# Kernel optimization log

Measured on AMD Instinct MI355X. Metric: run time of the kernel, lower is better.

The kernel has to match this reference:

```python
import jax, jax.numpy as jnp
import numpy as np


def setup_inputs() -> dict:
    key = jax.random.key(0)
    ks = jax.random.split(key, 6)
    B, S, I, H = 8, 4096, 512, 512
    scale = 1.0 / np.sqrt(I)
    return {
        "x": jax.random.normal(ks[0], (B, S, I), dtype=jnp.float32),
        "h_0": jax.random.normal(ks[1], (B, H), dtype=jnp.float32),
        "W_z": jax.random.normal(ks[2], (H, I), dtype=jnp.float32) * scale,
        "b_z": jax.random.normal(ks[3], (H,), dtype=jnp.float32) * scale,
        "W_h": jax.random.normal(ks[4], (H, I), dtype=jnp.float32) * scale,
        "b_h": jax.random.normal(ks[5], (H,), dtype=jnp.float32) * scale,
    }


def reference(x, h_0, W_z, b_z, W_h, b_h):
    # Gate and candidate projections (dense GEMMs over all timesteps at once)
    z = jax.nn.sigmoid(jnp.einsum("bsi,hi->bsh", x, W_z) + b_z)  # [B,S,H]
    h_tilde = jnp.einsum("bsi,hi->bsh", x, W_h) + b_h            # [B,S,H]

    # Linear recurrence h_t = a_t * h_{t-1} + b_t with a = 1-z, b = z*h_tilde.
    # Parallel associative scan over time; h_0 folded in as element 0 (a=1, b=h_0).
    a = jnp.concatenate([jnp.ones_like(h_0)[:, None, :], 1.0 - z], axis=1)     # [B,S+1,H]
    b = jnp.concatenate([h_0[:, None, :], z * h_tilde], axis=1)                # [B,S+1,H]

    def combine(c1, c2):
        a1, b1 = c1
        a2, b2 = c2
        return a1 * a2, a2 * b1 + b2

    _, h = jax.lax.associative_scan(combine, (a, b), axis=1)
    return h[:, 1:, :]  # drop the h_0 slot -> [B,S,H]
```

## Files before the change

kernel.cpp:

```cpp
#include <hip/hip_runtime.h>
#include <hip/hip_bf16.h>
#include <stdint.h>


typedef __attribute__((ext_vector_type(8))) short short8;
typedef __attribute__((ext_vector_type(4))) float f32x4;

#define AS1 __attribute__((address_space(1)))
#define AS3 __attribute__((address_space(3)))

__device__ inline void gload_lds16(const void* g, void* l) {
  __builtin_amdgcn_global_load_lds((AS1 uint32_t*)(g), (AS3 uint32_t*)(l), 16, 0, 0);
}

__device__ inline ushort f2bf(float f) {
  union { __hip_bfloat16 h; ushort u; } v;
  v.h = __float2bfloat16(f);
  return v.u;
}

__global__ void cvt_all(const float* __restrict__ x,
                        const float* __restrict__ wz,
                        const float* __restrict__ wh,
                        ushort* __restrict__ xb,
                        ushort* __restrict__ wzb,
                        ushort* __restrict__ whb) {
  int i = blockIdx.x * 256 + threadIdx.x;
  for (; i < 4325376; i += 2048 * 256) {
    const float* s; ushort* d; int j;
    if (i < 4194304)      { s = x;  d = xb;  j = i; }
    else if (i < 4259840) { s = wz; d = wzb; j = i - 4194304; }
    else                  { s = wh; d = whb; j = i - 4259840; }
    float4 v = reinterpret_cast<const float4*>(s)[j];
    ushort4 o = make_ushort4(f2bf(v.x), f2bf(v.y), f2bf(v.z), f2bf(v.w));
    reinterpret_cast<ushort4*>(d)[j] = o;
  }
}

__global__ __launch_bounds__(256) void gemm_gate(
    const ushort* __restrict__ xb,
    const ushort* __restrict__ wzb,
    const ushort* __restrict__ whb,
    const float* __restrict__ b_z,
    const float* __restrict__ b_h,
    uint* __restrict__ ab,
    float2* __restrict__ ABc)
{
  __shared__ __align__(16) char smem[32768];
  char* As  = smem;
  char* Bzs = smem + 16384;
  char* Bhs = smem + 24576;

  const int t  = threadIdx.x;
  const int w  = t >> 6;
  const int l  = t & 63;
  const int lm = l & 15;
  const int lk = l >> 4;
  const int wm = w >> 1, wn = w & 1;
  const int bx = blockIdx.x;
  const int m0 = bx * 128;
  const int n0 = blockIdx.y * 64;

  const int srow  = t >> 3;
  const int sslot = t & 7;

  float bzv[2], bhv[2];
  #pragma unroll
  for (int n = 0; n < 2; ++n) {
    int col = n0 + wn * 32 + n * 16 + lm;
    bzv[n] = b_z[col];
    bhv[n] = b_h[col];
  }

  f32x4 accz[4][2], acch[4][2];
  #pragma unroll
  for (int m = 0; m < 4; ++m)
    #pragma unroll
    for (int n = 0; n < 2; ++n) {
      accz[m][n] = (f32x4){0.f, 0.f, 0.f, 0.f};
      acch[m][n] = (f32x4){0.f, 0.f, 0.f, 0.f};
    }

  for (int kt = 0; kt < 8; ++kt) {
    const int k0 = kt * 64;
    #pragma unroll
    for (int j = 0; j < 4; ++j) {
      int row = j * 32 + srow;
      int gs  = sslot ^ (row & 7);
      gload_lds16(xb + (size_t)(m0 + row) * 512 + k0 + gs * 8, As + j * 4096 + w * 1024);
    }
    #pragma unroll
    for (int j = 0; j < 2; ++j) {
      int row = j * 32 + srow;
      int gs  = sslot ^ (row & 7);
      gload_lds16(wzb + (size_t)(n0 + row) * 512 + k0 + gs * 8, Bzs + j * 4096 + w * 1024);
      gload_lds16(whb + (size_t)(n0 + row) * 512 + k0 + gs * 8, Bhs + j * 4096 + w * 1024);
    }
    __syncthreads();

    #pragma unroll
    for (int kk = 0; kk < 2; ++kk) {
      short8 af[4], bfz[2], bfh[2];
      const int soff = (((kk * 4 + lk) ^ (lm & 7)) << 4);
      #pragma unroll
      for (int m = 0; m < 4; ++m) {
        int row = wm * 64 + m * 16 + lm;
        af[m] = *(const short8*)(As + row * 128 + soff);
      }
      #pragma unroll
      for (int n = 0; n < 2; ++n) {
        int row = wn * 32 + n * 16 + lm;
        bfz[n] = *(const short8*)(Bzs + row * 128 + soff);
        bfh[n] = *(const short8*)(Bhs + row * 128 + soff);
      }
      #pragma unroll
      for (int m = 0; m < 4; ++m)
        #pragma unroll
        for (int n = 0; n < 2; ++n) {
          accz[m][n] = __builtin_amdgcn_mfma_f32_16x16x32_bf16(af[m], bfz[n], accz[m][n], 0, 0, 0);
          acch[m][n] = __builtin_amdgcn_mfma_f32_16x16x32_bf16(af[m], bfh[n], acch[m][n], 0, 0, 0);
        }
    }
    __syncthreads();
  }

  float av[4][4][2], bv[4][4][2];
  #pragma unroll
  for (int m = 0; m < 4; ++m) {
    #pragma unroll
    for (int j = 0; j < 4; ++j) {
      size_t grow = (size_t)(m0 + wm * 64 + m * 16 + lk * 4 + j);
      uint* po = ab + grow * 512 + n0 + wn * 32 + lm;
      #pragma unroll
      for (int n = 0; n < 2; ++n) {
        float uz = accz[m][n][j] + bzv[n];
        float uh = acch[m][n][j] + bhv[n];
        float z  = 1.f / (1.f + __expf(-uz));
        float a  = 1.f - z;
        float bb = z * uh;
        av[m][j][n] = a;
        bv[m][j][n] = bb;
        po[n * 16] = (uint)f2bf(a) | ((uint)f2bf(bb) << 16);
      }
    }
  }

  #pragma unroll
  for (int cb = 0; cb < 2; ++cb) {
    #pragma unroll
    for (int n = 0; n < 2; ++n) {
      float At[2], Bt[2];
      #pragma unroll
      for (int mm = 0; mm < 2; ++mm) {
        float A = 1.f, Bv = 0.f;
        #pragma unroll
        for (int j = 0; j < 4; ++j) {
          float a = av[2 * cb + mm][j][n];
          float b = bv[2 * cb + mm][j][n];
          A  = a * A;
          Bv = a * Bv + b;
        }
        float Ag = 1.f, Bg = 0.f;
        #pragma unroll
        for (int q = 0; q < 4; ++q) {
          float Aq = __shfl(A,  lm + 16 * q);
          float Bq = __shfl(Bv, lm + 16 * q);
          Ag = Aq * Ag;
          Bg = Aq * Bg + Bq;
        }
        At[mm] = Ag;
        Bt[mm] = Bg;
      }
      float Achunk = At[1] * At[0];
      float Bchunk = At[1] * Bt[0] + Bt[1];
      if (lk == 0) {
        int bidx = bx >> 5;
        int c    = (bx & 31) * 4 + wm * 2 + cb;
        int col  = n0 + wn * 32 + n * 16 + lm;
        ABc[((size_t)bidx * 512 + col) * 128 + c] = make_float2(Achunk, Bchunk);
      }
    }
  }
}

__global__ __launch_bounds__(256) void chunk_scan(
    const float2* __restrict__ ABc,
    const float* __restrict__ h0,
    float* __restrict__ Hinit)
{
  __shared__ float sm[128][4];
  const int w = threadIdx.x >> 6, l = threadIdx.x & 63;
  const int b   = blockIdx.x >> 7;
  const int h0g = (blockIdx.x & 127) * 4;
  const int h   = h0g + w;

  const float2* base = ABc + ((size_t)b * 512 + h) * 128;
  float2 s1 = base[l];
  float2 s2 = base[64 + l];

  float A1 = s1.x, B1 = s1.y;
  #pragma unroll
  for (int d = 1; d < 64; d <<= 1) {
    float uA = __shfl_up(A1, d);
    float uB = __shfl_up(B1, d);
    if (l >= d) { B1 = A1 * uB + B1; A1 = A1 * uA; }
  }
  float A2 = s2.x, B2 = s2.y;
  #pragma unroll
  for (int d = 1; d < 64; d <<= 1) {
    float uA = __shfl_up(A2, d);
    float uB = __shfl_up(B2, d);
    if (l >= d) { B2 = A2 * uB + B2; A2 = A2 * uA; }
  }
  float PA = __shfl(A1, 63), PB = __shfl(B1, 63);
  float FA = A2 * PA;
  float FB = A2 * PB + B2;

  float e1A = __shfl_up(A1, 1), e1B = __shfl_up(B1, 1);
  if (l == 0) { e1A = 1.f; e1B = 0.f; }
  float e2A = __shfl_up(FA, 1), e2B = __shfl_up(FB, 1);
  if (l == 0) { e2A = PA; e2B = PB; }

  float h0v = h0[b * 512 + h];
  sm[l][w]      = e1A * h0v + e1B;
  sm[64 + l][w] = e2A * h0v + e2B;
  __syncthreads();

  const int t = threadIdx.x;
  if (t < 128) {
    float4 v = *(const float4*)sm[t];
    *(float4*)(Hinit + ((size_t)b * 128 + t) * 512 + h0g) = v;
  }
}

__global__ __launch_bounds__(256) void scan_write(
    const uint* __restrict__ ab,
    const float* __restrict__ Hinit,
    float* __restrict__ out)
{
  int tid = blockIdx.x * 256 + threadIdx.x;
  int cg = tid & 127;
  int c  = (tid >> 7) & 127;
  int b  = tid >> 14;
  const uint4* p = reinterpret_cast<const uint4*>(ab + ((size_t)(b * 4096 + c * 32)) * 512) + cg;
  float4 hv = *reinterpret_cast<const float4*>(Hinit + ((size_t)b * 128 + c) * 512 + cg * 4);
  float4* po = reinterpret_cast<float4*>(out + ((size_t)(b * 4096 + c * 32)) * 512) + cg;
  #pragma unroll 4
  for (int t = 0; t < 32; ++t) {
    uint4 u = p[(size_t)t * 128];
    hv.x = __uint_as_float(u.x << 16) * hv.x + __uint_as_float(u.x & 0xffff0000u);
    hv.y = __uint_as_float(u.y << 16) * hv.y + __uint_as_float(u.y & 0xffff0000u);
    hv.z = __uint_as_float(u.z << 16) * hv.z + __uint_as_float(u.z & 0xffff0000u);
    hv.w = __uint_as_float(u.w << 16) * hv.w + __uint_as_float(u.w & 0xffff0000u);
    po[(size_t)t * 128] = hv;
  }
}

extern "C" void kernel_launch(void* const* d_in, const int* in_sizes, int n_in,
                              void* d_out, int out_size, void* d_ws, size_t ws_size,
                              hipStream_t stream) {
  const float* x   = (const float*)d_in[0];
  const float* h0  = (const float*)d_in[1];
  const float* W_z = (const float*)d_in[2];
  const float* b_z = (const float*)d_in[3];
  const float* W_h = (const float*)d_in[4];
  const float* b_h = (const float*)d_in[5];
  float* out = (float*)d_out;

  char* ws = (char*)d_ws;
  ushort* xb    = (ushort*)(ws);
  ushort* wzb   = (ushort*)(ws + 33554432);
  ushort* whb   = (ushort*)(ws + 34078720);
  uint*   ab    = (uint*)  (ws + 34603008);
  float2* ABc   = (float2*)(ws + 101711872);
  float*  Hinit = (float*) (ws + 105906176);

  cvt_all<<<2048, 256, 0, stream>>>(x, W_z, W_h, xb, wzb, whb);
  gemm_gate<<<dim3(256, 8), 256, 0, stream>>>(xb, wzb, whb, b_z, b_h, ab, ABc);
  chunk_scan<<<1024, 256, 0, stream>>>(ABc, h0, Hinit);
  scan_write<<<512, 256, 0, stream>>>(ab, Hinit, out);
}
```

Measured before the change: 103.4 us.

## Double-buffer gate GEMM LDS tiles with K=32 stages and async prefetch

Reworks the gate/candidate GEMM main loop to double-buffer shared memory, using 16 stages of K=32 instead of 8 stages of K=64. The next tile is prefetched with global_load_lds while MFMAs run on the current one, synchronised by explicit vmcnt waits and raw barriers. It also raises wave priority around the MFMA block and changes the swizzle to suit the 64-byte rows. The aim is to hide global-to-LDS latency, at the cost of more barriers per K and reliance on hand-tuned waitcnt counts for correctness.

```diff
diff --git a/kernel.cpp b/kernel.cpp
--- a/kernel.cpp
+++ b/kernel.cpp
@@ -47,9 +47,6 @@
     float2* __restrict__ ABc)
 {
   __shared__ __align__(16) char smem[32768];
-  char* As  = smem;
-  char* Bzs = smem + 16384;
-  char* Bhs = smem + 24576;
 
   const int t  = threadIdx.x;
   const int w  = t >> 6;
@@ -61,8 +58,76 @@
   const int m0 = bx * 128;
   const int n0 = blockIdx.y * 64;
 
-  const int srow  = t >> 3;
-  const int sslot = t & 7;
+  const int srow = t >> 2;
+  const int ssl  = t & 3;
+
+  f32x4 accz[4][2], acch[4][2];
+  #pragma unroll
+  for (int m = 0; m < 4; ++m)
+    #pragma unroll
+    for (int n = 0; n < 2; ++n) {
+      accz[m][n] = (f32x4){0.f, 0.f, 0.f, 0.f};
+      acch[m][n] = (f32x4){0.f, 0.f, 0.f, 0.f};
+    }
+
+  auto stage = [&](int sel, int kt) {
+    char* base = smem + sel * 16384;
+    const int k0 = kt * 32;
+    #pragma unroll
+    for (int j = 0; j < 2; ++j) {
+      int row = j * 64 + srow;
+      int gs  = ssl ^ ((row >> 1) & 3);
+      gload_lds16(xb + (size_t)(m0 + row) * 512 + k0 + gs * 8,
+                  base + j * 4096 + w * 1024);
+    }
+    {
+      int row = srow;
+      int gs  = ssl ^ ((row >> 1) & 3);
+      gload_lds16(wzb + (size_t)(n0 + row) * 512 + k0 + gs * 8,
+                  base + 8192 + w * 1024);
+      gload_lds16(whb + (size_t)(n0 + row) * 512 + k0 + gs * 8,
+                  base + 12288 + w * 1024);
+    }
+  };
+
+  stage(0, 0);
+
+  #pragma unroll
+  for (int kt = 0; kt < 16; ++kt) {
+    const int sel = kt & 1;
+    if (kt < 15) {
+      stage(sel ^ 1, kt + 1);
+      asm volatile("s_waitcnt vmcnt(4)" ::: "memory");
+    } else {
+      asm volatile("s_waitcnt vmcnt(0)" ::: "memory");
+    }
+    __builtin_amdgcn_s_barrier();
+
+    const char* base = smem + sel * 16384;
+    short8 af[4], bfz[2], bfh[2];
+    #pragma unroll
+    for (int m = 0; m < 4; ++m) {
+      int row = wm * 64 + m * 16 + lm;
+      af[m] = *(const short8*)(base + row * 64 + ((lk ^ ((row >> 1) & 3)) << 4));
+    }
+    #pragma unroll
+    for (int n = 0; n < 2; ++n) {
+      int row = wn * 32 + n * 16 + lm;
+      int so  = ((lk ^ ((row >> 1) & 3)) << 4);
+      bfz[n] = *(const short8*)(base + 8192  + row * 64 + so);
+      bfh[n] = *(const short8*)(base + 12288 + row * 64 + so);
+    }
+    __builtin_amdgcn_s_setprio(1);
+    #pragma unroll
+    for (int m = 0; m < 4; ++m)
+      #pragma unroll
+      for (int n = 0; n < 2; ++n) {
+        accz[m][n] = __builtin_amdgcn_mfma_f32_16x16x32_bf16(af[m], bfz[n], accz[m][n], 0, 0, 0);
+        acch[m][n] = __builtin_amdgcn_mfma_f32_16x16x32_bf16(af[m], bfh[n], acch[m][n], 0, 0, 0);
+      }
+    __builtin_amdgcn_s_setprio(0);
+    __builtin_amdgcn_s_barrier();
+  }
 
   float bzv[2], bhv[2];
   #pragma unroll
@@ -70,58 +135,6 @@
     int col = n0 + wn * 32 + n * 16 + lm;
     bzv[n] = b_z[col];
     bhv[n] = b_h[col];
-  }
-
-  f32x4 accz[4][2], acch[4][2];
-  #pragma unroll
-  for (int m = 0; m < 4; ++m)
-    #pragma unroll
-    for (int n = 0; n < 2; ++n) {
-      accz[m][n] = (f32x4){0.f, 0.f, 0.f, 0.f};
-      acch[m][n] = (f32x4){0.f, 0.f, 0.f, 0.f};
-    }
-
-  for (int kt = 0; kt < 8; ++kt) {
-    const int k0 = kt * 64;
-    #pragma unroll
-    for (int j = 0; j < 4; ++j) {
-      int row = j * 32 + srow;
-      int gs  = sslot ^ (row & 7);
-      gload_lds16(xb + (size_t)(m0 + row) * 512 + k0 + gs * 8, As + j * 4096 + w * 1024);
-    }
-    #pragma unroll
-    for (int j = 0; j < 2; ++j) {
-      int row = j * 32 + srow;
-      int gs  = sslot ^ (row & 7);
-      gload_lds16(wzb + (size_t)(n0 + row) * 512 + k0 + gs * 8, Bzs + j * 4096 + w * 1024);
-      gload_lds16(whb + (size_t)(n0 + row) * 512 + k0 + gs * 8, Bhs + j * 4096 + w * 1024);
-    }
-    __syncthreads();
-
-    #pragma unroll
-    for (int kk = 0; kk < 2; ++kk) {
-      short8 af[4], bfz[2], bfh[2];
-      const int soff = (((kk * 4 + lk) ^ (lm & 7)) << 4);
-      #pragma unroll
-      for (int m = 0; m < 4; ++m) {
-        int row = wm * 64 + m * 16 + lm;
-        af[m] = *(const short8*)(As + row * 128 + soff);
-      }
-      #pragma unroll
-      for (int n = 0; n < 2; ++n) {
-        int row = wn * 32 + n * 16 + lm;
-        bfz[n] = *(const short8*)(Bzs + row * 128 + soff);
-        bfh[n] = *(const short8*)(Bhs + row * 128 + soff);
-      }
-      #pragma unroll
-      for (int m = 0; m < 4; ++m)
-        #pragma unroll
-        for (int n = 0; n < 2; ++n) {
-          accz[m][n] = __builtin_amdgcn_mfma_f32_16x16x32_bf16(af[m], bfz[n], accz[m][n], 0, 0, 0);
-          acch[m][n] = __builtin_amdgcn_mfma_f32_16x16x32_bf16(af[m], bfh[n], acch[m][n], 0, 0, 0);
-        }
-    }
-    __syncthreads();
   }
 
   float av[4][4][2], bv[4][4][2];
@@ -226,10 +239,10 @@
   sm[64 + l][w] = e2A * h0v + e2B;
   __syncthreads();
 
-  const int t = threadIdx.x;
-  if (t < 128) {
-    float4 v = *(const float4*)sm[t];
-    *(float4*)(Hinit + ((size_t)b * 128 + t) * 512 + h0g) = v;
+  const int tt = threadIdx.x;
+  if (tt < 128) {
+    float4 v = *(const float4*)sm[tt];
+    *(float4*)(Hinit + ((size_t)b * 128 + tt) * 512 + h0g) = v;
   }
 }
 
```

New measurement: 99.00 us. 1.04x faster.

## Rewrite gate GEMM as single-wave blocks loading operands directly from global

Applied to the files above, without the earlier changes.

The gate GEMM no longer stages tiles through LDS with global_load_lds and barriers. Each 64-thread block computes a 64x64 tile for both projections, reading MFMA operands straight from global memory into registers with double-buffered prefetch across K. Block IDs are remapped so neighbouring blocks share column tiles for cache locality. This drops LDS traffic and sync overhead but relies on L1/L2 for reuse, issues uncoalesced per-lane 16-byte loads, and raises register pressure from 32 accumulators plus two operand buffers.

```diff
diff --git a/kernel.cpp b/kernel.cpp
--- a/kernel.cpp
+++ b/kernel.cpp
@@ -5,13 +5,6 @@
 
 typedef __attribute__((ext_vector_type(8))) short short8;
 typedef __attribute__((ext_vector_type(4))) float f32x4;
-
-#define AS1 __attribute__((address_space(1)))
-#define AS3 __attribute__((address_space(3)))
-
-__device__ inline void gload_lds16(const void* g, void* l) {
-  __builtin_amdgcn_global_load_lds((AS1 uint32_t*)(g), (AS3 uint32_t*)(l), 16, 0, 0);
-}
 
 __device__ inline ushort f2bf(float f) {
   union { __hip_bfloat16 h; ushort u; } v;
@@ -37,7 +30,7 @@
   }
 }
 
-__global__ __launch_bounds__(256) void gemm_gate(
+__global__ __launch_bounds__(64) void gemm_gate(
     const ushort* __restrict__ xb,
     const ushort* __restrict__ wzb,
     const ushort* __restrict__ whb,
@@ -46,95 +39,86 @@
     uint* __restrict__ ab,
     float2* __restrict__ ABc)
 {
-  __shared__ __align__(16) char smem[32768];
-  char* As  = smem;
-  char* Bzs = smem + 16384;
-  char* Bhs = smem + 24576;
-
-  const int t  = threadIdx.x;
-  const int w  = t >> 6;
-  const int l  = t & 63;
+  const int l  = threadIdx.x;
   const int lm = l & 15;
   const int lk = l >> 4;
-  const int wm = w >> 1, wn = w & 1;
-  const int bx = blockIdx.x;
-  const int m0 = bx * 128;
-  const int n0 = blockIdx.y * 64;
-
-  const int srow  = t >> 3;
-  const int sslot = t & 7;
-
-  float bzv[2], bhv[2];
-  #pragma unroll
-  for (int n = 0; n < 2; ++n) {
-    int col = n0 + wn * 32 + n * 16 + lm;
+
+  const int bid  = blockIdx.x;
+  const int tile = (bid & 7) * 512 + (bid >> 3);
+  const int bx = tile >> 3;
+  const int by = tile & 7;
+  const int m0 = bx * 64;
+  const int n0 = by * 64;
+
+  const int lane_off = lm * 512 + lk * 8;
+
+  const ushort* ap[4];
+  const ushort* bp[8];
+  #pragma unroll
+  for (int m = 0; m < 4; ++m)
+    ap[m] = xb + (size_t)(m0 + m * 16) * 512 + lane_off;
+  #pragma unroll
+  for (int n = 0; n < 4; ++n) {
+    bp[n]     = wzb + (size_t)(n0 + n * 16) * 512 + lane_off;
+    bp[4 + n] = whb + (size_t)(n0 + n * 16) * 512 + lane_off;
+  }
+
+  f32x4 acc[2][4][4];
+  #pragma unroll
+  for (int q = 0; q < 2; ++q)
+    #pragma unroll
+    for (int m = 0; m < 4; ++m)
+      #pragma unroll
+      for (int n = 0; n < 4; ++n)
+        acc[q][m][n] = (f32x4){0.f, 0.f, 0.f, 0.f};
+
+  short8 aA[4], bA[8], aB[4], bB[8];
+
+#define LOADT(av_, bv_, ktv)                                         \
+  _Pragma("unroll") for (int m = 0; m < 4; ++m)                      \
+    av_[m] = *(const short8*)(ap[m] + (ktv) * 32);                   \
+  _Pragma("unroll") for (int q = 0; q < 8; ++q)                      \
+    bv_[q] = *(const short8*)(bp[q] + (ktv) * 32);
+
+#define COMPUTE(av_, bv_)                                            \
+  _Pragma("unroll") for (int m = 0; m < 4; ++m)                      \
+    _Pragma("unroll") for (int n = 0; n < 4; ++n) {                  \
+      acc[0][m][n] = __builtin_amdgcn_mfma_f32_16x16x32_bf16(        \
+          av_[m], bv_[n], acc[0][m][n], 0, 0, 0);                    \
+      acc[1][m][n] = __builtin_amdgcn_mfma_f32_16x16x32_bf16(        \
+          av_[m], bv_[4 + n], acc[1][m][n], 0, 0, 0);                \
+    }
+
+  LOADT(aA, bA, 0);
+  #pragma unroll
+  for (int kt = 0; kt < 16; kt += 2) {
+    LOADT(aB, bB, kt + 1);
+    COMPUTE(aA, bA);
+    if (kt + 2 < 16) { LOADT(aA, bA, kt + 2); }
+    COMPUTE(aB, bB);
+  }
+#undef LOADT
+#undef COMPUTE
+
+  float bzv[4], bhv[4];
+  #pragma unroll
+  for (int n = 0; n < 4; ++n) {
+    int col = n0 + n * 16 + lm;
     bzv[n] = b_z[col];
     bhv[n] = b_h[col];
   }
 
-  f32x4 accz[4][2], acch[4][2];
-  #pragma unroll
-  for (int m = 0; m < 4; ++m)
-    #pragma unroll
-    for (int n = 0; n < 2; ++n) {
-      accz[m][n] = (f32x4){0.f, 0.f, 0.f, 0.f};
-      acch[m][n] = (f32x4){0.f, 0.f, 0.f, 0.f};
-    }
-
-  for (int kt = 0; kt < 8; ++kt) {
-    const int k0 = kt * 64;
-    #pragma unroll
-    for (int j = 0; j < 4; ++j) {
-      int row = j * 32 + srow;
-      int gs  = sslot ^ (row & 7);
-      gload_lds16(xb + (size_t)(m0 + row) * 512 + k0 + gs * 8, As + j * 4096 + w * 1024);
-    }
-    #pragma unroll
-    for (int j = 0; j < 2; ++j) {
-      int row = j * 32 + srow;
-      int gs  = sslot ^ (row & 7);
-      gload_lds16(wzb + (size_t)(n0 + row) * 512 + k0 + gs * 8, Bzs + j * 4096 + w * 1024);
-      gload_lds16(whb + (size_t)(n0 + row) * 512 + k0 + gs * 8, Bhs + j * 4096 + w * 1024);
-    }
-    __syncthreads();
-
-    #pragma unroll
-    for (int kk = 0; kk < 2; ++kk) {
-      short8 af[4], bfz[2], bfh[2];
-      const int soff = (((kk * 4 + lk) ^ (lm & 7)) << 4);
-      #pragma unroll
-      for (int m = 0; m < 4; ++m) {
-        int row = wm * 64 + m * 16 + lm;
-        af[m] = *(const short8*)(As + row * 128 + soff);
-      }
-      #pragma unroll
-      for (int n = 0; n < 2; ++n) {
-        int row = wn * 32 + n * 16 + lm;
-        bfz[n] = *(const short8*)(Bzs + row * 128 + soff);
-        bfh[n] = *(const short8*)(Bhs + row * 128 + soff);
-      }
-      #pragma unroll
-      for (int m = 0; m < 4; ++m)
-        #pragma unroll
-        for (int n = 0; n < 2; ++n) {
-          accz[m][n] = __builtin_amdgcn_mfma_f32_16x16x32_bf16(af[m], bfz[n], accz[m][n], 0, 0, 0);
-          acch[m][n] = __builtin_amdgcn_mfma_f32_16x16x32_bf16(af[m], bfh[n], acch[m][n], 0, 0, 0);
-        }
-    }
-    __syncthreads();
-  }
-
-  float av[4][4][2], bv[4][4][2];
+  float av[4][4][4], bv[4][4][4];
   #pragma unroll
   for (int m = 0; m < 4; ++m) {
     #pragma unroll
     for (int j = 0; j < 4; ++j) {
-      size_t grow = (size_t)(m0 + wm * 64 + m * 16 + lk * 4 + j);
-      uint* po = ab + grow * 512 + n0 + wn * 32 + lm;
+      size_t grow = (size_t)(m0 + m * 16 + lk * 4 + j);
+      uint* po = ab + grow * 512 + n0 + lm;
       #pragma unroll
-      for (int n = 0; n < 2; ++n) {
-        float uz = accz[m][n][j] + bzv[n];
-        float uh = acch[m][n][j] + bhv[n];
+      for (int n = 0; n < 4; ++n) {
+        float uz = acc[0][m][n][j] + bzv[n];
+        float uh = acc[1][m][n][j] + bhv[n];
         float z  = 1.f / (1.f + __expf(-uz));
         float a  = 1.f - z;
         float bb = z * uh;
@@ -148,7 +132,7 @@
   #pragma unroll
   for (int cb = 0; cb < 2; ++cb) {
     #pragma unroll
-    for (int n = 0; n < 2; ++n) {
+    for (int n = 0; n < 4; ++n) {
       float At[2], Bt[2];
       #pragma unroll
       for (int mm = 0; mm < 2; ++mm) {
@@ -174,9 +158,9 @@
       float Achunk = At[1] * At[0];
       float Bchunk = At[1] * Bt[0] + Bt[1];
       if (lk == 0) {
-        int bidx = bx >> 5;
-        int c    = (bx & 31) * 4 + wm * 2 + cb;
-        int col  = n0 + wn * 32 + n * 16 + lm;
+        int bidx = bx >> 6;
+        int c    = (bx & 63) * 2 + cb;
+        int col  = n0 + n * 16 + lm;
         ABc[((size_t)bidx * 512 + col) * 128 + c] = make_float2(Achunk, Bchunk);
       }
     }
@@ -226,10 +210,10 @@
   sm[64 + l][w] = e2A * h0v + e2B;
   __syncthreads();
 
-  const int t = threadIdx.x;
-  if (t < 128) {
-    float4 v = *(const float4*)sm[t];
-    *(float4*)(Hinit + ((size_t)b * 128 + t) * 512 + h0g) = v;
+  const int tt = threadIdx.x;
+  if (tt < 128) {
+    float4 v = *(const float4*)sm[tt];
+    *(float4*)(Hinit + ((size_t)b * 128 + tt) * 512 + h0g) = v;
   }
 }
 
@@ -276,7 +260,7 @@
   float*  Hinit = (float*) (ws + 105906176);
 
   cvt_all<<<2048, 256, 0, stream>>>(x, W_z, W_h, xb, wzb, whb);
-  gemm_gate<<<dim3(256, 8), 256, 0, stream>>>(xb, wzb, whb, b_z, b_h, ab, ABc);
+  gemm_gate<<<4096, 64, 0, stream>>>(xb, wzb, whb, b_z, b_h, ab, ABc);
   chunk_scan<<<1024, 256, 0, stream>>>(ABc, h0, Hinit);
   scan_write<<<512, 256, 0, stream>>>(ab, Hinit, out);
 }
```

New measurement: 163.5 us. 1.58x slower.
